# Performance work log

Hardware: AMD Instinct MI355X
Metric: run time of the kernel (lower is better)

Reference implementation:

```python
import jax, jax.numpy as jnp
import numpy as np

N_E, E_DIM, BETA = 8192, 512, 0.25


def setup_inputs() -> dict:
    key = jax.random.key(0)
    k1, k2 = jax.random.split(key)
    z = jax.random.normal(k1, (16, 1024, E_DIM), dtype=jnp.float32)
    # embedding initialized uniform(-1/n_e, 1/n_e)
    emb_w = jax.random.uniform(k2, (N_E, E_DIM), dtype=jnp.float32,
                               minval=-1.0 / N_E, maxval=1.0 / N_E)
    return {"z": z, "emb_w": emb_w}


def reference(z, emb_w):
    B, T, D = z.shape
    zf = z.reshape(-1, D)  # [BT, D]
    # squared-distance matrix: ||z||^2 + ||e||^2 - 2 z e^T  -> [BT, n_e]
    d = (jnp.sum(zf * zf, axis=1, keepdims=True)
         + jnp.sum(emb_w * emb_w, axis=1)
         - 2.0 * jnp.einsum('bd,nd->bn', zf, emb_w))
    idx = jnp.argmin(d, axis=1)  # [BT]
    z_q = emb_w[idx].reshape(z.shape)  # [B, T, D]
    # legacy=False: beta * commit + codebook term
    loss = (BETA * jnp.mean((jax.lax.stop_gradient(z_q) - z) ** 2)
            + jnp.mean((z_q - jax.lax.stop_gradient(z)) ** 2))
    # straight-through: value equals z_q
    z_q_st = z + jax.lax.stop_gradient(z_q - z)
    idx_out = idx.reshape(B, T)
    v = jnp.var(idx_out.astype(jnp.float32))
    return z_q_st, loss, idx_out, v
```

## Files before the change

kernel.cpp:

```cpp
#include <hip/hip_runtime.h>


#define BT   16384
#define DIMS 512
#define NE   8192
#define NS   4
#define BN   256
#define NTPB (NE / NS / BN)
#define NSTEPS 64

#define LOSS_OFF 8388608
#define IDX_OFF  8388609
#define V_OFF    8404993

#define BEST_OFF  0
#define ENORM_OFF 131072
#define SUMS_OFF  163840
#define CNT_OFF   163864

typedef __attribute__((ext_vector_type(8))) short short8;
typedef __attribute__((ext_vector_type(4))) float floatx4;

#define AS1(p) ((const __attribute__((address_space(1))) void*)(p))
#define AS3(p) ((__attribute__((address_space(3))) void*)(p))

__device__ __forceinline__ unsigned f2bf(float f) {
    unsigned u = __builtin_bit_cast(unsigned, f);
    u += 0x7FFFu + ((u >> 16) & 1u);
    return u >> 16;
}

__global__ __launch_bounds__(256) void prep_kernel(
    const float* __restrict__ z, const float* __restrict__ emb,
    ushort* __restrict__ zh, ushort* __restrict__ ehh,
    float* __restrict__ enorm, unsigned long long* __restrict__ best,
    double* __restrict__ sums, unsigned* __restrict__ counter)
{
    const int lane = threadIdx.x & 63, w = threadIdx.x >> 6;
    const int b = blockIdx.x;
    if (b < NE / 4) {
        const int row = b * 4 + w;
        const float4* p = (const float4*)(emb + (size_t)row * DIMS + lane * 8);
        float4 a = p[0], bb = p[1];
        uint4 h;
        h.x = f2bf(a.x) | (f2bf(a.y) << 16);
        h.y = f2bf(a.z) | (f2bf(a.w) << 16);
        h.z = f2bf(bb.x) | (f2bf(bb.y) << 16);
        h.w = f2bf(bb.z) | (f2bf(bb.w) << 16);
        *(uint4*)(ehh + (size_t)row * DIMS + lane * 8) = h;
        float s = a.x*a.x + a.y*a.y + a.z*a.z + a.w*a.w
                + bb.x*bb.x + bb.y*bb.y + bb.z*bb.z + bb.w*bb.w;
        #pragma unroll
        for (int off = 32; off > 0; off >>= 1) s += __shfl_down(s, off, 64);
        if (lane == 0) enorm[row] = s;
    } else {
        const int row = (b - NE / 4) * 4 + w;
        const float4* p = (const float4*)(z + (size_t)row * DIMS + lane * 8);
        float4 a = p[0], bb = p[1];
        uint4 h;
        h.x = f2bf(a.x) | (f2bf(a.y) << 16);
        h.y = f2bf(a.z) | (f2bf(a.w) << 16);
        h.z = f2bf(bb.x) | (f2bf(bb.y) << 16);
        h.w = f2bf(bb.z) | (f2bf(bb.w) << 16);
        *(uint4*)(zh + (size_t)row * DIMS + lane * 8) = h;
    }
    const int gid = b * 256 + threadIdx.x;
    if (gid < BT) best[gid] = 0xFFFFFFFFFFFFFFFFULL;
    if (gid == 0) { sums[0] = 0.0; sums[1] = 0.0; sums[2] = 0.0; *counter = 0u; }
}


__device__ __forceinline__ void dsr_fence() {
    asm volatile("s_waitcnt lgkmcnt(0)" ::: "memory");
    __builtin_amdgcn_sched_barrier(0);
}

#define DSR8(dst, IDX) do {                                                    \
    unsigned addr_ = (unsigned)(size_t)AS3(&lds[IDX]);                         \
    asm volatile("ds_read_b128 %0, %1" : "=v"(dst) : "v"(addr_));              \
} while (0)

#define LGK(N_) do {                                                           \
    asm volatile("s_waitcnt lgkmcnt(" #N_ ")" ::: "memory");                   \
    __builtin_amdgcn_sched_barrier(0);                                         \
} while (0)

#define CL4(J_, BIDX_)                                                         \
    _Pragma("unroll")                                                          \
    for (int mi = 0; mi < 4; mi++)                                             \
        acc[mi][J_] = __builtin_amdgcn_mfma_f32_16x16x32_bf16(                 \
            a[mi], b[BIDX_], acc[mi][J_], 0, 0, 0);

#define STAGE_A(SA_, H_) do {                                                  \
    const int sa_ = (SA_);                                                     \
    const int sc_ = sa_ & 63;                                                  \
    const unsigned al_ = (unsigned)(sa_ & 1) * 32768u                          \
                       + (unsigned)((((H_) * 128) + w * 8) * 64);              \
    const ushort* g_ = zA + (size_t)((H_) * 128) * DIMS + soff                 \
                     + ((sc_ & 7) * 64);                                       \
    __builtin_amdgcn_global_load_lds(AS1(g_), AS3(&lds[al_]), 16, 0, 0);       \
    __builtin_amdgcn_global_load_lds(AS1(g_ + (size_t)64 * DIMS),              \
                                     AS3(&lds[al_ + 64 * 64]), 16, 0, 0);      \
} while (0)

#define STAGE_B(SB_, H_) do {                                                  \
    const int sb_ = (SB_);                                                     \
    const int sc_ = sb_ & 63;                                                  \
    const unsigned bl_ = 16384u + (unsigned)(sb_ & 1) * 32768u                 \
                       + (unsigned)((((H_) * 128) + w * 8) * 64);              \
    const ushort* g_ = eh + (size_t)(nsN + (sc_ >> 3) * 256 + (H_) * 128) * DIMS \
                     + soff + ((sc_ & 7) * 64);                                \
    __builtin_amdgcn_global_load_lds(AS1(g_), AS3(&lds[bl_]), 16, 0, 0);       \
    __builtin_amdgcn_global_load_lds(AS1(g_ + (size_t)64 * DIMS),              \
                                     AS3(&lds[bl_ + 64 * 64]), 16, 0, 0);      \
} while (0)

#define STEP(S_, AB_, TM_) do {                                                \
    const int s_ = (S_);                                                       \
    short8 a[4], b[8];                                                         \
                                                                       \
    _Pragma("unroll") for (int mi = 0; mi < 4; mi++)                           \
        DSR8(a[mi], (AB_) + aro + mi * 1024 + pxo0);                           \
    _Pragma("unroll") for (int j = 0; j < 4; j++)                              \
        DSR8(b[j], 16384u + (AB_) + bro + j * 1024 + pxo0);                    \
    STAGE_B(s_ + 1, 0);                                                        \
    __builtin_amdgcn_s_setprio(1);                                             \
    LGK(3); CL4(0, 0); LGK(2); CL4(1, 1); LGK(1); CL4(2, 2); LGK(0); CL4(3, 3);\
    __builtin_amdgcn_s_setprio(0);                                             \
                                                                       \
    _Pragma("unroll") for (int j = 0; j < 4; j++)                              \
        DSR8(b[4 + j], 16384u + (AB_) + bro + (4 + j) * 1024 + pxo0);          \
    _Pragma("unroll") for (int j = 0; j < 4; j++)                              \
        DSR8(b[j], 16384u + (AB_) + bro + j * 1024 + pxo1);                    \
    STAGE_B(s_ + 1, 1);                                                        \
    __builtin_amdgcn_s_setprio(1);                                             \
    LGK(7); CL4(4, 4); LGK(6); CL4(5, 5); LGK(5); CL4(6, 6); LGK(4); CL4(7, 7);\
    __builtin_amdgcn_s_setprio(0);                                             \
                                                                       \
    _Pragma("unroll") for (int mi = 0; mi < 4; mi++)                           \
        DSR8(a[mi], (AB_) + aro + mi * 1024 + pxo1);                           \
    _Pragma("unroll") for (int j = 0; j < 4; j++)                              \
        DSR8(b[4 + j], 16384u + (AB_) + bro + (4 + j) * 1024 + pxo1);          \
    __builtin_amdgcn_s_setprio(1);                                             \
    LGK(4); CL4(0, 0); CL4(1, 1); CL4(2, 2); CL4(3, 3);                        \
    __builtin_amdgcn_s_setprio(0);                                             \
    __builtin_amdgcn_sched_barrier(0);                                         \
    __builtin_amdgcn_s_barrier();            \
                                                                       \
    STAGE_A(s_ + 2, 0); STAGE_A(s_ + 2, 1);                                    \
    __builtin_amdgcn_s_setprio(1);                                             \
    LGK(3); CL4(4, 4); LGK(2); CL4(5, 5); LGK(1); CL4(6, 6); LGK(0); CL4(7, 7);\
    __builtin_amdgcn_s_setprio(0);                                             \
    __builtin_amdgcn_sched_barrier(0);                                         \
    if ((TM_) == 0) asm volatile("s_waitcnt vmcnt(4)" ::: "memory");           \
    __builtin_amdgcn_s_barrier();                                              \
} while (0)

__global__ __launch_bounds__(512, 2) void argmin_mfma(
    const ushort* __restrict__ zh, const ushort* __restrict__ eh,
    const float* __restrict__ enorm, unsigned long long* __restrict__ best)
{
    __shared__ __align__(16) ushort lds[69632];
    float* elds = (float*)&lds[65536];

    const int t = threadIdx.x;
    const int w = t >> 6, lane = t & 63;
    const int quad = lane >> 4, l15 = lane & 15;

    const int d = blockIdx.x;
    const int xcd = d & 7, slot = d >> 3;
    const int ns = xcd >> 1;
    const int mt = slot * 2 + (xcd & 1);
    const int m0 = mt * 256;
    const int nsN = ns * (NTPB * BN);

    const int wrow = (w & 3) * 64;
    const int wcol = (w >> 2) * 128;

    {
        float4 v = *(const float4*)(enorm + nsN + t * 4);
        *(float4*)(elds + t * 4) = v;
    }
    __syncthreads();

    const int l8 = lane >> 3, c8 = lane & 7;
    const int chunk = c8 ^ l8;
    const int soff = (w * 8 + l8) * DIMS + chunk * 8;
    const ushort* zA = zh + (size_t)m0 * DIMS;

    const int pxo0 = (quad ^ (l15 & 7)) * 8;
    const int pxo1 = ((4 + quad) ^ (l15 & 7)) * 8;
    const int aro = (wrow + l15) * 64;
    const int bro = (wcol + l15) * 64;

    floatx4 acc[4][8];
    #pragma unroll
    for (int mi = 0; mi < 4; mi++)
        #pragma unroll
        for (int nj = 0; nj < 8; nj++)
            acc[mi][nj] = (floatx4){0.f, 0.f, 0.f, 0.f};

    float bs[16];
    int   bn_[16];
    #pragma unroll
    for (int k = 0; k < 16; k++) { bs[k] = 3.4e38f; bn_[k] = 0; }

    STAGE_A(0, 0); STAGE_A(0, 1);
    STAGE_B(0, 0); STAGE_B(0, 1);
    STAGE_A(1, 0); STAGE_A(1, 1);
    asm volatile("s_waitcnt vmcnt(4)" ::: "memory");
    __builtin_amdgcn_s_barrier();

    for (int sp = 0; sp < NSTEPS; sp += 2) {
        STEP(sp, 0u, 0);
        STEP(sp + 1, 32768u, (sp == NSTEPS - 2) ? 2 : 0);

        if ((sp & 7) == 6) {
            const int nt = sp >> 3;
            const int eb = nt * 256 + wcol + l15;
            const int nbase = nsN + eb;
            float en[8];
            #pragma unroll
            for (int nj = 0; nj < 8; nj++) {
                unsigned addr_ = (unsigned)(size_t)AS3(&elds[eb + nj * 16]);
                asm volatile("ds_read_b32 %0, %1" : "=v"(en[nj]) : "v"(addr_));
            }
            dsr_fence();
            #pragma unroll
            for (int nj = 0; nj < 8; nj++) {
                const int n = nbase + nj * 16;
                #pragma unroll
                for (int mi = 0; mi < 4; mi++) {
                    #pragma unroll
                    for (int r = 0; r < 4; r++) {
                        const int k = mi * 4 + r;
                        const float sc = fmaf(-2.0f, acc[mi][nj][r], en[nj]);
                        if (sc < bs[k]) { bs[k] = sc; bn_[k] = n; }
                    }
                    acc[mi][nj] = (floatx4){0.f, 0.f, 0.f, 0.f};
                }
            }
        }
    }

    asm volatile("s_waitcnt vmcnt(0)" ::: "memory");

    #pragma unroll
    for (int mi = 0; mi < 4; mi++)
        #pragma unroll
        for (int r = 0; r < 4; r++) {
            const int k = mi * 4 + r;
            unsigned su = __builtin_bit_cast(unsigned, bs[k]);
            su = (su & 0x80000000u) ? ~su : (su | 0x80000000u);
            unsigned long long key = ((unsigned long long)su << 32) | (unsigned)bn_[k];
            #pragma unroll
            for (int off = 1; off < 16; off <<= 1) {
                unsigned long long o = __shfl_xor(key, off, 64);
                key = (o < key) ? o : key;
            }
            if (l15 == 0) atomicMin(&best[m0 + wrow + mi * 16 + quad * 4 + r], key);
        }
}

__global__ __launch_bounds__(256) void gather_loss_kernel(
    const float* __restrict__ z, const float* __restrict__ emb,
    const unsigned long long* __restrict__ best,
    float* __restrict__ out, double* __restrict__ sums, unsigned* __restrict__ counter)
{
    __shared__ int sIdx[32];
    __shared__ double red[4];
    const int t = threadIdx.x;
    const int row0 = blockIdx.x * 32;
    double myIdxSum = 0.0, myIdxSq = 0.0;
    if (t < 32) {
        int row = row0 + t;
        int idx = (int)(unsigned)(best[row] & 0xFFFFFFFFULL);
        sIdx[t] = idx;
        out[IDX_OFF + row] = (float)idx;
        myIdxSum = (double)idx;
        myIdxSq = (double)idx * (double)idx;
    }
    __syncthreads();
    double acc = 0.0;
    #pragma unroll 4
    for (int i = 0; i < 16; i++) {
        int e = i * 1024 + t * 4;
        int rl = e >> 9;
        int c = e & 511;
        int idx = sIdx[rl];
        float4 zv = *(const float4*)(z + (size_t)(row0 + rl) * DIMS + c);
        float4 ev = *(const float4*)(emb + (size_t)idx * DIMS + c);
        *(float4*)(out + (size_t)(row0 + rl) * DIMS + c) = ev;
        float dx = zv.x - ev.x, dy = zv.y - ev.y;
        float dz = zv.z - ev.z, dw = zv.w - ev.w;
        acc += (double)(dx * dx + dy * dy) + (double)(dz * dz + dw * dw);
    }
    const int lane = t & 63, wv = t >> 6;
    #pragma unroll
    for (int off = 32; off > 0; off >>= 1) {
        acc      += __shfl_down(acc, off, 64);
        myIdxSum += __shfl_down(myIdxSum, off, 64);
        myIdxSq  += __shfl_down(myIdxSq, off, 64);
    }
    if (lane == 0) red[wv] = acc;
    __syncthreads();
    if (t == 0) {
        double tot = red[0] + red[1] + red[2] + red[3];
        atomicAdd(&sums[0], tot);
        atomicAdd(&sums[1], myIdxSum);
        atomicAdd(&sums[2], myIdxSq);
        __threadfence();
        unsigned old = atomicAdd(counter, 1u);
        if (old == gridDim.x - 1) {
            __threadfence();
            double s0 = atomicAdd(&sums[0], 0.0);
            double s1 = atomicAdd(&sums[1], 0.0);
            double s2 = atomicAdd(&sums[2], 0.0);
            out[LOSS_OFF] = (float)(1.25 * s0 / (double)((size_t)BT * DIMS));
            double m = s1 / (double)BT;
            out[V_OFF] = (float)(s2 / (double)BT - m * m);
        }
    }
}

extern "C" void kernel_launch(void* const* d_in, const int* in_sizes, int n_in,
                              void* d_out, int out_size, void* d_ws, size_t ws_size,
                              hipStream_t stream) {
    const float* z = (const float*)d_in[0];
    const float* emb = (const float*)d_in[1];
    float* out = (float*)d_out;
    char* ws = (char*)d_ws;
    unsigned long long* best = (unsigned long long*)(ws + BEST_OFF);
    float* enorm  = (float*)(ws + ENORM_OFF);
    double* sums  = (double*)(ws + SUMS_OFF);
    unsigned* counter = (unsigned*)(ws + CNT_OFF);

    ushort* zh = (ushort*)out;
    ushort* ehh = zh + (size_t)BT * DIMS;

    hipLaunchKernelGGL(prep_kernel, dim3(NE / 4 + BT / 4), dim3(256), 0, stream,
                       z, emb, zh, ehh, enorm, best, sums, counter);
    hipLaunchKernelGGL(argmin_mfma, dim3(256), dim3(512), 0, stream,
                       zh, ehh, enorm, best);
    hipLaunchKernelGGL(gather_loss_kernel, dim3(BT / 32), dim3(256), 0, stream,
                       z, emb, best, out, sums, counter);
}
```

Before: 244.2 us.

## Restructure MFMA step to drop the mid-step barrier and prefetch A one step ahead

Each step now issues both halves of the B prefetch up front. A is prefetched for the next step rather than two steps ahead, and both K-halves of A are held in registers so the MFMA sequence runs as four groups without an internal barrier. The aim is to remove one workgroup barrier per step and simplify the LDS double-buffer schedule. In exchange, the end of each step now waits on all outstanding global loads (vmcnt(0)). That shortens the prefetch distance and may expose global-to-LDS latency that the deeper A prefetch used to hide.

```diff
diff --git a/kernel.cpp b/kernel.cpp
--- a/kernel.cpp
+++ b/kernel.cpp
@@ -85,11 +85,11 @@
     __builtin_amdgcn_sched_barrier(0);                                         \
 } while (0)
 
-#define CL4(J_, BIDX_)                                                         \
+#define CL4(J_, BIDX_, KK_)                                                    \
     _Pragma("unroll")                                                          \
     for (int mi = 0; mi < 4; mi++)                                             \
         acc[mi][J_] = __builtin_amdgcn_mfma_f32_16x16x32_bf16(                 \
-            a[mi], b[BIDX_], acc[mi][J_], 0, 0, 0);
+            a[mi][KK_], b[BIDX_], acc[mi][J_], 0, 0, 0);
 
 #define STAGE_A(SA_, H_) do {                                                  \
     const int sa_ = (SA_);                                                     \
@@ -117,42 +117,43 @@
 
 #define STEP(S_, AB_, TM_) do {                                                \
     const int s_ = (S_);                                                       \
-    short8 a[4], b[8];                                                         \
+    short8 a[4][2], b[4];                                                      \
                                                                        \
     _Pragma("unroll") for (int mi = 0; mi < 4; mi++)                           \
-        DSR8(a[mi], (AB_) + aro + mi * 1024 + pxo0);                           \
+        DSR8(a[mi][0], (AB_) + aro + mi * 1024 + pxo0);                        \
     _Pragma("unroll") for (int j = 0; j < 4; j++)                              \
         DSR8(b[j], 16384u + (AB_) + bro + j * 1024 + pxo0);                    \
-    STAGE_B(s_ + 1, 0);                                                        \
+    STAGE_B(s_ + 1, 0); STAGE_B(s_ + 1, 1);                                    \
     __builtin_amdgcn_s_setprio(1);                                             \
-    LGK(3); CL4(0, 0); LGK(2); CL4(1, 1); LGK(1); CL4(2, 2); LGK(0); CL4(3, 3);\
+    LGK(3); CL4(0, 0, 0); LGK(2); CL4(1, 1, 0);                                \
+    LGK(1); CL4(2, 2, 0); LGK(0); CL4(3, 3, 0);                                \
     __builtin_amdgcn_s_setprio(0);                                             \
                                                                        \
     _Pragma("unroll") for (int j = 0; j < 4; j++)                              \
-        DSR8(b[4 + j], 16384u + (AB_) + bro + (4 + j) * 1024 + pxo0);          \
+        DSR8(b[j], 16384u + (AB_) + bro + (4 + j) * 1024 + pxo0);              \
+    _Pragma("unroll") for (int mi = 0; mi < 4; mi++)                           \
+        DSR8(a[mi][1], (AB_) + aro + mi * 1024 + pxo1);                        \
+    STAGE_A(s_ + 1, 0); STAGE_A(s_ + 1, 1);                                    \
+    __builtin_amdgcn_s_setprio(1);                                             \
+    LGK(7); CL4(4, 0, 0); LGK(6); CL4(5, 1, 0);                                \
+    LGK(5); CL4(6, 2, 0); LGK(4); CL4(7, 3, 0);                                \
+    __builtin_amdgcn_s_setprio(0);                                             \
+                                                                       \
     _Pragma("unroll") for (int j = 0; j < 4; j++)                              \
         DSR8(b[j], 16384u + (AB_) + bro + j * 1024 + pxo1);                    \
-    STAGE_B(s_ + 1, 1);                                                        \
     __builtin_amdgcn_s_setprio(1);                                             \
-    LGK(7); CL4(4, 4); LGK(6); CL4(5, 5); LGK(5); CL4(6, 6); LGK(4); CL4(7, 7);\
+    LGK(3); CL4(0, 0, 1); LGK(2); CL4(1, 1, 1);                                \
+    LGK(1); CL4(2, 2, 1); LGK(0); CL4(3, 3, 1);                                \
     __builtin_amdgcn_s_setprio(0);                                             \
                                                                        \
-    _Pragma("unroll") for (int mi = 0; mi < 4; mi++)                           \
-        DSR8(a[mi], (AB_) + aro + mi * 1024 + pxo1);                           \
     _Pragma("unroll") for (int j = 0; j < 4; j++)                              \
-        DSR8(b[4 + j], 16384u + (AB_) + bro + (4 + j) * 1024 + pxo1);          \
+        DSR8(b[j], 16384u + (AB_) + bro + (4 + j) * 1024 + pxo1);              \
     __builtin_amdgcn_s_setprio(1);                                             \
-    LGK(4); CL4(0, 0); CL4(1, 1); CL4(2, 2); CL4(3, 3);                        \
+    LGK(3); CL4(4, 0, 1); LGK(2); CL4(5, 1, 1);                                \
+    LGK(1); CL4(6, 2, 1); LGK(0); CL4(7, 3, 1);                                \
     __builtin_amdgcn_s_setprio(0);                                             \
     __builtin_amdgcn_sched_barrier(0);                                         \
-    __builtin_amdgcn_s_barrier();            \
-                                                                       \
-    STAGE_A(s_ + 2, 0); STAGE_A(s_ + 2, 1);                                    \
-    __builtin_amdgcn_s_setprio(1);                                             \
-    LGK(3); CL4(4, 4); LGK(2); CL4(5, 5); LGK(1); CL4(6, 6); LGK(0); CL4(7, 7);\
-    __builtin_amdgcn_s_setprio(0);                                             \
-    __builtin_amdgcn_sched_barrier(0);                                         \
-    if ((TM_) == 0) asm volatile("s_waitcnt vmcnt(4)" ::: "memory");           \
+    if ((TM_) == 0) asm volatile("s_waitcnt vmcnt(0)" ::: "memory");           \
     __builtin_amdgcn_s_barrier();                                              \
 } while (0)
 
@@ -207,8 +208,7 @@
 
     STAGE_A(0, 0); STAGE_A(0, 1);
     STAGE_B(0, 0); STAGE_B(0, 1);
-    STAGE_A(1, 0); STAGE_A(1, 1);
-    asm volatile("s_waitcnt vmcnt(4)" ::: "memory");
+    asm volatile("s_waitcnt vmcnt(0)" ::: "memory");
     __builtin_amdgcn_s_barrier();
 
     for (int sp = 0; sp < NSTEPS; sp += 2) {
```

New measurement: 246.9 us. No clear change (+1.1%).
